# Kernel optimization log

Hardware: AMD Instinct MI355X
Metric: run time of the kernel (lower is better)

The kernel has to match this reference:

```python
import jax, jax.numpy as jnp
import numpy as np

B, C, L = 128, 1, 4096


def setup_inputs() -> dict:
    key = jax.random.key(0)
    x_0 = jax.random.normal(key, (B, C, L), dtype=jnp.float32)
    return {"x_0": x_0}


def reference(x_0):
    # Original: per-sample F.conv1d(x, flip(x), padding=L-1).
    # Cross-correlation with a flipped kernel == full linear convolution:
    #   out[b, t] = sum_c sum_i x[b,c,i] * x[b,c,t-i],  t in [0, 2L-2]
    # Vectorized over batch and channels via vmap; summed over channels
    # (conv1d contracts input channels against the weight's channel dim).
    conv = jax.vmap(jax.vmap(lambda a: jnp.convolve(a, a, mode='full')))(x_0)  # [B, C, 2L-1]
    return conv.sum(axis=1)[:, None, :]  # [B, 1, 2L-1]
```

## Files before the change

kernel.cpp:

```cpp
#include <hip/hip_runtime.h>

#define LL    4096
#define OUTL  8191
#define PAD   1024
#define NTOT  6144
#define NPAIR 3072
#define CSTR  3848
#define REVBASE 15392
#define LDS_DW  (REVBASE + 3072)

typedef short v8s __attribute__((ext_vector_type(8)));
typedef float v4f __attribute__((ext_vector_type(4)));

__device__ __forceinline__ unsigned bf16b(float f) {
    unsigned u = __builtin_bit_cast(unsigned, f);
    u += 0x7fff + ((u >> 16) & 1);
    return u >> 16;
}
__device__ __forceinline__ int physdw(int r, int p) { return r * CSTR + p + 2 * (p >> 3); }
__device__ __forceinline__ int revdw(int g) { return REVBASE + 4 * (g ^ ((g >> 3) & 7)); }

struct Frag { uint2 a0l, a0h, a1l, a1h; uint4 b0, b1; };

__global__ __launch_bounds__(512)
void selfconv_mfma2(const float* __restrict__ xg, float* __restrict__ outg) {
    __shared__ unsigned lds[LDS_DW];
    const int tid = threadIdx.x;
    const int b   = blockIdx.x >> 1;
    const int h   = blockIdx.x & 1;
    const float* __restrict__ xb = xg + b * LL;

    for (int r = 0; r < 4; ++r)
        for (int p = tid; p < NPAIR; p += 512) {
            int e0 = 2 * p + r - PAD;
            int e1 = e0 + 1;
            float f0 = (e0 >= 0 && e0 < LL) ? xb[e0] : 0.f;
            float f1 = (e1 >= 0 && e1 < LL) ? xb[e1] : 0.f;
            lds[physdw(r, p)] = bf16b(f0) | (bf16b(f1) << 16);
        }
    for (int g = tid; g < NTOT / 8; g += 512) {
        unsigned w[4];
#pragma unroll
        for (int d = 0; d < 4; ++d) {
            int xlo = 6143 - 8 * g - 2 * d - PAD;
            int xhi = xlo - 1;
            float flo = (xlo >= 0 && xlo < LL) ? xb[xlo] : 0.f;
            float fhi = (xhi >= 0 && xhi < LL) ? xb[xhi] : 0.f;
            w[d] = bf16b(flo) | (bf16b(fhi) << 16);
        }
        *(uint4*)&lds[revdw(g)] = uint4{w[0], w[1], w[2], w[3]};
    }
    __syncthreads();

    const int wv   = tid >> 6;
    const int lane = tid & 63;
    const int ln16 = lane & 15;
    const int q    = lane >> 4;
    const int tw   = wv & 3;
    const int half = wv >> 2;

    const int perm0[4] = {0, 3, 5, 6};
    const int perm1[4] = {1, 2, 4, 7};
    const int M  = h ? perm1[tw] : perm0[tw];
    const int T0 = M << 10;

    int mn = 0x7fffffff, mx = -0x7fffffff;
#pragma unroll
    for (int u = 0; u < 2; ++u)
#pragma unroll
        for (int v = 0; v < 2; ++v) {
            int base = T0 + 256 * u + 512 * v;
            int iLo = base - (LL - 1); if (iLo < 0) iLo = 0;
            int iHi = base + 255;      if (iHi > LL - 1) iHi = LL - 1;
            int a = iLo - 256 * u; if (a < mn) mn = a;
            int c2 = iHi - 256 * u; if (c2 > mx) mx = c2;
        }
    const int base_   = mn - 15;
    const int i0start = base_ - ((base_ - 1) & 7);
    const int nch     = ((mx - i0start) >> 5) + 1;
    const int nw      = (nch - half + 1) >> 1;

    const int i0w = i0start + 32 * half;
    int uA = i0w + ln16 + 8 * q + PAD;
    int rA = uA & 3, pA = (uA >> 2) << 1;
    int awA0 = physdw(rA, pA), awA1 = physdw(rA, pA + 2);
    int gB = ((5119 - T0 + i0w) >> 3) - 2 * ln16 + q;

    v4f acc00{0,0,0,0}, acc01{0,0,0,0}, acc10{0,0,0,0}, acc11{0,0,0,0};

    auto loadF = [&](Frag& F) {
        F.a0l = *(const uint2*)&lds[awA0];
        F.a0h = *(const uint2*)&lds[awA1];
        F.a1l = *(const uint2*)&lds[awA0 + 160];
        F.a1h = *(const uint2*)&lds[awA1 + 160];
        int d0 = revdw(gB);
        F.b0 = *(const uint4*)&lds[d0];
        F.b1 = *(const uint4*)&lds[d0 - 256];
    };
    auto adv = [&]() { awA0 += 40; awA1 += 40; gB += 8; };
    auto mk8_2 = [](uint2 lo, uint2 hi) {
        union { unsigned u[4]; v8s s; } z;
        z.u[0] = lo.x; z.u[1] = lo.y; z.u[2] = hi.x; z.u[3] = hi.y; return z.s;
    };
    auto mk8_4 = [](uint4 v) {
        union { unsigned u[4]; v8s s; } z;
        z.u[0] = v.x; z.u[1] = v.y; z.u[2] = v.z; z.u[3] = v.w; return z.s;
    };
    auto compute = [&](const Frag& F) {
        v8s A0 = mk8_2(F.a0l, F.a0h);
        v8s A1 = mk8_2(F.a1l, F.a1h);
        v8s B0 = mk8_4(F.b0);
        v8s B1 = mk8_4(F.b1);
        acc00 = __builtin_amdgcn_mfma_f32_16x16x32_bf16(A0, B0, acc00, 0, 0, 0);
        acc01 = __builtin_amdgcn_mfma_f32_16x16x32_bf16(A0, B1, acc01, 0, 0, 0);
        acc10 = __builtin_amdgcn_mfma_f32_16x16x32_bf16(A1, B0, acc10, 0, 0, 0);
        acc11 = __builtin_amdgcn_mfma_f32_16x16x32_bf16(A1, B1, acc11, 0, 0, 0);
    };

    Frag F0, F1;
    if (nw > 0) loadF(F0);
    adv();
    int it = 0;
    for (; it + 2 <= nw; it += 2) {
        loadF(F1); adv();
        compute(F0);
        loadF(F0); adv();
        compute(F1);
    }
    if (it < nw) compute(F0);

    __syncthreads();
    float* fs = (float*)lds;
    const int sb = (tw * 64 + lane) * 20;
    if (half == 1) {
        *(v4f*)&fs[sb]      = acc00;
        *(v4f*)&fs[sb + 4]  = acc10;
        *(v4f*)&fs[sb + 8]  = acc01;
        *(v4f*)&fs[sb + 12] = acc11;
    }
    __syncthreads();
    if (half == 0) {
        acc00 += *(const v4f*)&fs[sb];
        acc10 += *(const v4f*)&fs[sb + 4];
        acc01 += *(const v4f*)&fs[sb + 8];
        acc11 += *(const v4f*)&fs[sb + 12];
        float* __restrict__ ob = outg + b * OUTL;
        const v4f* accs[4] = {&acc00, &acc10, &acc01, &acc11};
#pragma unroll
        for (int uv = 0; uv < 4; ++uv) {
            int u = uv & 1, v = uv >> 1;
            int t = T0 + 256 * u + 512 * v + 4 * q + 16 * ln16;
            v4f a = *accs[uv];
#pragma unroll
            for (int r2 = 0; r2 < 4; ++r2)
                if (t + r2 < OUTL) ob[t + r2] = a[r2];
        }
    }
}

extern "C" void kernel_launch(void* const* d_in, const int* in_sizes, int n_in,
                              void* d_out, int out_size, void* d_ws, size_t ws_size,
                              hipStream_t stream) {
    const float* x = (const float*)d_in[0];
    float* out = (float*)d_out;
    selfconv_mfma2<<<dim3(256), dim3(512), 0, stream>>>(x, out);
}
```

Measured before the change: 70.62 us.

## Widen per-wave output tile to 2048 and split reduction across four waves

Each block now covers a 2048-wide output range with 256 threads, 512 blocks, instead of 1024-wide ranges with 512 threads. Each wave keeps eight MFMA accumulators rather than four, so every loaded A fragment is reused across four B fragments. The reduction dimension is split over all four waves, and three waves' partial sums go through LDS before the final store. The load pipeline is triple-buffered with clamped chunk indices, and LDS staging is trimmed to a smaller padded window loaded with wider stores. This raises register pressure and makes the cross-wave reduction larger.

```diff
diff --git a/kernel.cpp b/kernel.cpp
--- a/kernel.cpp
+++ b/kernel.cpp
@@ -1,13 +1,14 @@
 #include <hip/hip_runtime.h>
 
-#define LL    4096
-#define OUTL  8191
-#define PAD   1024
-#define NTOT  6144
-#define NPAIR 3072
-#define CSTR  3848
-#define REVBASE 15392
-#define LDS_DW  (REVBASE + 3072)
+#define LL     4096
+#define OUTL   8191
+#define FPAD   272
+#define NPAIRF 2340
+#define CSTRF  2952
+#define REVB   11808
+#define BTOP   5895
+#define NG     968
+#define LDS_DW 15680
 
 typedef short v8s __attribute__((ext_vector_type(8)));
 typedef float v4f __attribute__((ext_vector_type(4)));
@@ -17,32 +18,40 @@
     u += 0x7fff + ((u >> 16) & 1);
     return u >> 16;
 }
-__device__ __forceinline__ int physdw(int r, int p) { return r * CSTR + p + 2 * (p >> 3); }
-__device__ __forceinline__ int revdw(int g) { return REVBASE + 4 * (g ^ ((g >> 3) & 7)); }
+__device__ __forceinline__ int physdw(int r, int p) { return r * CSTRF + p + 2 * (p >> 3); }
+__device__ __forceinline__ int revdw(int g) { return REVB + 4 * (g ^ ((g >> 3) & 7)); }
 
-struct Frag { uint2 a0l, a0h, a1l, a1h; uint4 b0, b1; };
+struct Frag { uint2 a0l, a0h, a1l, a1h; uint4 b0, b1, b2, b3; };
 
-__global__ __launch_bounds__(512)
-void selfconv_mfma2(const float* __restrict__ xg, float* __restrict__ outg) {
+__global__ __launch_bounds__(256)
+void selfconv_mfma3(const float* __restrict__ xg, float* __restrict__ outg) {
     __shared__ unsigned lds[LDS_DW];
     const int tid = threadIdx.x;
-    const int b   = blockIdx.x >> 1;
-    const int h   = blockIdx.x & 1;
+    const int blk = blockIdx.x;
+    const int h2 = blk >> 8;
+    const int b  = (blk & 255) >> 1;
+    const int rg = (blk & 1) + 2 * h2;
+    const int T0 = rg << 11;
     const float* __restrict__ xb = xg + b * LL;
 
     for (int r = 0; r < 4; ++r)
-        for (int p = tid; p < NPAIR; p += 512) {
-            int e0 = 2 * p + r - PAD;
-            int e1 = e0 + 1;
-            float f0 = (e0 >= 0 && e0 < LL) ? xb[e0] : 0.f;
-            float f1 = (e1 >= 0 && e1 < LL) ? xb[e1] : 0.f;
-            lds[physdw(r, p)] = bf16b(f0) | (bf16b(f1) << 16);
+        for (int pp = tid; pp < NPAIRF / 2; pp += 256) {
+            int p = 2 * pp;
+            int e = 4 * pp + r - FPAD;
+            float f0 = (e >= 0 && e < LL) ? xb[e] : 0.f;
+            float f1 = (e + 1 >= 0 && e + 1 < LL) ? xb[e + 1] : 0.f;
+            float f2 = (e + 2 >= 0 && e + 2 < LL) ? xb[e + 2] : 0.f;
+            float f3 = (e + 3 >= 0 && e + 3 < LL) ? xb[e + 3] : 0.f;
+            uint2 w;
+            w.x = bf16b(f0) | (bf16b(f1) << 16);
+            w.y = bf16b(f2) | (bf16b(f3) << 16);
+            *(uint2*)&lds[physdw(r, p)] = w;
         }
-    for (int g = tid; g < NTOT / 8; g += 512) {
+    for (int g = tid; g < NG; g += 256) {
         unsigned w[4];
 #pragma unroll
         for (int d = 0; d < 4; ++d) {
-            int xlo = 6143 - 8 * g - 2 * d - PAD;
+            int xlo = BTOP - (8 * g + 2 * d);
             int xhi = xlo - 1;
             float flo = (xlo >= 0 && xlo < LL) ? xb[xlo] : 0.f;
             float fhi = (xhi >= 0 && xhi < LL) ? xb[xhi] : 0.f;
@@ -56,19 +65,12 @@
     const int lane = tid & 63;
     const int ln16 = lane & 15;
     const int q    = lane >> 4;
-    const int tw   = wv & 3;
-    const int half = wv >> 2;
-
-    const int perm0[4] = {0, 3, 5, 6};
-    const int perm1[4] = {1, 2, 4, 7};
-    const int M  = h ? perm1[tw] : perm0[tw];
-    const int T0 = M << 10;
 
     int mn = 0x7fffffff, mx = -0x7fffffff;
 #pragma unroll
     for (int u = 0; u < 2; ++u)
 #pragma unroll
-        for (int v = 0; v < 2; ++v) {
+        for (int v = 0; v < 4; ++v) {
             int base = T0 + 256 * u + 512 * v;
             int iLo = base - (LL - 1); if (iLo < 0) iLo = 0;
             int iHi = base + 255;      if (iHi > LL - 1) iHi = LL - 1;
@@ -78,82 +80,93 @@
     const int base_   = mn - 15;
     const int i0start = base_ - ((base_ - 1) & 7);
     const int nch     = ((mx - i0start) >> 5) + 1;
-    const int nw      = (nch - half + 1) >> 1;
+    const int nw      = (nch - wv + 3) >> 2;
+    const int cmax    = nw - 1;
+    const int i0w     = i0start + 32 * wv;
 
-    const int i0w = i0start + 32 * half;
-    int uA = i0w + ln16 + 8 * q + PAD;
+    int uA = i0w + ln16 + 8 * q + FPAD;
     int rA = uA & 3, pA = (uA >> 2) << 1;
-    int awA0 = physdw(rA, pA), awA1 = physdw(rA, pA + 2);
-    int gB = ((5119 - T0 + i0w) >> 3) - 2 * ln16 + q;
+    const int awA0 = physdw(rA, pA), awA1 = physdw(rA, pA + 2);
+    const int gB0 = ((BTOP - T0 + i0w) >> 3) - 2 * ln16 + q;
 
-    v4f acc00{0,0,0,0}, acc01{0,0,0,0}, acc10{0,0,0,0}, acc11{0,0,0,0};
+    v4f acc00{0,0,0,0}, acc01{0,0,0,0}, acc02{0,0,0,0}, acc03{0,0,0,0};
+    v4f acc10{0,0,0,0}, acc11{0,0,0,0}, acc12{0,0,0,0}, acc13{0,0,0,0};
 
-    auto loadF = [&](Frag& F) {
-        F.a0l = *(const uint2*)&lds[awA0];
-        F.a0h = *(const uint2*)&lds[awA1];
-        F.a1l = *(const uint2*)&lds[awA0 + 160];
-        F.a1h = *(const uint2*)&lds[awA1 + 160];
-        int d0 = revdw(gB);
-        F.b0 = *(const uint4*)&lds[d0];
-        F.b1 = *(const uint4*)&lds[d0 - 256];
+    auto ld = [&](Frag& F, int c) {
+        int ic = c > cmax ? cmax : c;
+        int oA = 80 * ic;
+        F.a0l = *(const uint2*)&lds[awA0 + oA];
+        F.a0h = *(const uint2*)&lds[awA1 + oA];
+        F.a1l = *(const uint2*)&lds[awA0 + oA + 160];
+        F.a1h = *(const uint2*)&lds[awA1 + oA + 160];
+        int g = gB0 + 16 * ic;
+        F.b0 = *(const uint4*)&lds[revdw(g)];
+        F.b1 = *(const uint4*)&lds[revdw(g - 64)];
+        F.b2 = *(const uint4*)&lds[revdw(g - 128)];
+        F.b3 = *(const uint4*)&lds[revdw(g - 192)];
     };
-    auto adv = [&]() { awA0 += 40; awA1 += 40; gB += 8; };
-    auto mk8_2 = [](uint2 lo, uint2 hi) {
+    auto mk2 = [](uint2 lo, uint2 hi) {
         union { unsigned u[4]; v8s s; } z;
         z.u[0] = lo.x; z.u[1] = lo.y; z.u[2] = hi.x; z.u[3] = hi.y; return z.s;
     };
-    auto mk8_4 = [](uint4 v) {
+    auto mk4 = [](uint4 v) {
         union { unsigned u[4]; v8s s; } z;
         z.u[0] = v.x; z.u[1] = v.y; z.u[2] = v.z; z.u[3] = v.w; return z.s;
     };
-    auto compute = [&](const Frag& F) {
-        v8s A0 = mk8_2(F.a0l, F.a0h);
-        v8s A1 = mk8_2(F.a1l, F.a1h);
-        v8s B0 = mk8_4(F.b0);
-        v8s B1 = mk8_4(F.b1);
+    auto cmp = [&](const Frag& F) {
+        v8s A0 = mk2(F.a0l, F.a0h), A1 = mk2(F.a1l, F.a1h);
+        v8s B0 = mk4(F.b0), B1 = mk4(F.b1), B2 = mk4(F.b2), B3 = mk4(F.b3);
         acc00 = __builtin_amdgcn_mfma_f32_16x16x32_bf16(A0, B0, acc00, 0, 0, 0);
+        acc10 = __builtin_amdgcn_mfma_f32_16x16x32_bf16(A1, B0, acc10, 0, 0, 0);
         acc01 = __builtin_amdgcn_mfma_f32_16x16x32_bf16(A0, B1, acc01, 0, 0, 0);
-        acc10 = __builtin_amdgcn_mfma_f32_16x16x32_bf16(A1, B0, acc10, 0, 0, 0);
         acc11 = __builtin_amdgcn_mfma_f32_16x16x32_bf16(A1, B1, acc11, 0, 0, 0);
+        acc02 = __builtin_amdgcn_mfma_f32_16x16x32_bf16(A0, B2, acc02, 0, 0, 0);
+        acc12 = __builtin_amdgcn_mfma_f32_16x16x32_bf16(A1, B2, acc12, 0, 0, 0);
+        acc03 = __builtin_amdgcn_mfma_f32_16x16x32_bf16(A0, B3, acc03, 0, 0, 0);
+        acc13 = __builtin_amdgcn_mfma_f32_16x16x32_bf16(A1, B3, acc13, 0, 0, 0);
     };
 
-    Frag F0, F1;
-    if (nw > 0) loadF(F0);
-    adv();
-    int it = 0;
-    for (; it + 2 <= nw; it += 2) {
-        loadF(F1); adv();
-        compute(F0);
-        loadF(F0); adv();
-        compute(F1);
+    Frag F0, F1, F2;
+    ld(F0, 0); ld(F1, 1);
+    int c = 0;
+    for (; c + 3 <= nw; c += 3) {
+        ld(F2, c + 2); cmp(F0);
+        ld(F0, c + 3); cmp(F1);
+        ld(F1, c + 4); cmp(F2);
     }
-    if (it < nw) compute(F0);
+    if (c < nw)     cmp(F0);
+    if (c + 1 < nw) cmp(F1);
 
     __syncthreads();
     float* fs = (float*)lds;
-    const int sb = (tw * 64 + lane) * 20;
-    if (half == 1) {
-        *(v4f*)&fs[sb]      = acc00;
-        *(v4f*)&fs[sb + 4]  = acc10;
-        *(v4f*)&fs[sb + 8]  = acc01;
-        *(v4f*)&fs[sb + 12] = acc11;
+    if (wv > 0) {
+        int sb = ((wv - 1) * 64 + lane) * 36;
+        *(v4f*)&fs[sb]      = acc00; *(v4f*)&fs[sb + 4]  = acc10;
+        *(v4f*)&fs[sb + 8]  = acc01; *(v4f*)&fs[sb + 12] = acc11;
+        *(v4f*)&fs[sb + 16] = acc02; *(v4f*)&fs[sb + 20] = acc12;
+        *(v4f*)&fs[sb + 24] = acc03; *(v4f*)&fs[sb + 28] = acc13;
     }
     __syncthreads();
-    if (half == 0) {
-        acc00 += *(const v4f*)&fs[sb];
-        acc10 += *(const v4f*)&fs[sb + 4];
-        acc01 += *(const v4f*)&fs[sb + 8];
-        acc11 += *(const v4f*)&fs[sb + 12];
+    if (wv == 0) {
+#pragma unroll
+        for (int s = 0; s < 3; ++s) {
+            int sb = (s * 64 + lane) * 36;
+            acc00 += *(const v4f*)&fs[sb];      acc10 += *(const v4f*)&fs[sb + 4];
+            acc01 += *(const v4f*)&fs[sb + 8];  acc11 += *(const v4f*)&fs[sb + 12];
+            acc02 += *(const v4f*)&fs[sb + 16]; acc12 += *(const v4f*)&fs[sb + 20];
+            acc03 += *(const v4f*)&fs[sb + 24]; acc13 += *(const v4f*)&fs[sb + 28];
+        }
         float* __restrict__ ob = outg + b * OUTL;
-        const v4f* accs[4] = {&acc00, &acc10, &acc01, &acc11};
+        const v4f* accs[8] = {&acc00, &acc10, &acc01, &acc11,
+                              &acc02, &acc12, &acc03, &acc13};
 #pragma unroll
-        for (int uv = 0; uv < 4; ++uv) {
+        for (int uv = 0; uv < 8; ++uv) {
             int u = uv & 1, v = uv >> 1;
-            int t = T0 + 256 * u + 512 * v + 4 * q + 16 * ln16;
+            int tb = T0 + 256 * u + 512 * v + 4 * q + 16 * ln16;
             v4f a = *accs[uv];
 #pragma unroll
             for (int r2 = 0; r2 < 4; ++r2)
-                if (t + r2 < OUTL) ob[t + r2] = a[r2];
+                if (tb + r2 < OUTL) ob[tb + r2] = a[r2];
         }
     }
 }
@@ -163,5 +176,5 @@
                               hipStream_t stream) {
     const float* x = (const float*)d_in[0];
     float* out = (float*)d_out;
-    selfconv_mfma2<<<dim3(256), dim3(512), 0, stream>>>(x, out);
+    selfconv_mfma3<<<dim3(512), dim3(256), 0, stream>>>(x, out);
 }
```

After: 74.21 us. 1.05x slower.
